# Kernel tuning notes

Hardware: AMD Instinct MI355X
Metric: run time of the kernel (lower is better)

## Reference

```python
import jax, jax.numpy as jnp
import numpy as np

HIDDEN_D = 1024
MAP_D = 2048


def lstm_cell(x, h, c, W_ih, W_hh, b_ih, b_hh):
    # PyTorch LSTMCell: gates ordered (i, f, g, o)
    gates = x @ W_ih.T + b_ih + h @ W_hh.T + b_hh  # [1, 4H]
    i, f, g, o = jnp.split(gates, 4, axis=-1)
    i = jax.nn.sigmoid(i)
    f = jax.nn.sigmoid(f)
    g = jnp.tanh(g)
    o = jax.nn.sigmoid(o)
    c_new = f * c + i * g
    h_new = o * jnp.tanh(c_new)
    return h_new, c_new


def setup_inputs() -> dict:
    key = jax.random.key(0)
    ks = jax.random.split(key, 16)
    H = HIDDEN_D
    s = 1.0 / np.sqrt(H)  # PyTorch LSTMCell init scale
    inp = {
        "goal_point": jax.random.normal(ks[0], (2,), jnp.float32),
        "current_point": jax.random.normal(ks[1], (2,), jnp.float32),
        "map": jax.random.normal(ks[2], (1, MAP_D), jnp.float32),
        # lstm_map: input_size = MAP_D
        "W_ih_map": jax.random.uniform(ks[3], (4 * H, MAP_D), jnp.float32, -s, s),
        "W_hh_map": jax.random.uniform(ks[4], (4 * H, H), jnp.float32, -s, s),
        "b_ih_map": jax.random.uniform(ks[5], (4 * H,), jnp.float32, -s, s),
        "b_hh_map": jax.random.uniform(ks[6], (4 * H,), jnp.float32, -s, s),
        # lstm_points: input_size = 4
        "W_ih_pts": jax.random.uniform(ks[7], (4 * H, 4), jnp.float32, -s, s),
        "W_hh_pts": jax.random.uniform(ks[8], (4 * H, H), jnp.float32, -s, s),
        "b_ih_pts": jax.random.uniform(ks[9], (4 * H,), jnp.float32, -s, s),
        "b_hh_pts": jax.random.uniform(ks[10], (4 * H,), jnp.float32, -s, s),
        # lstm1: input_size = 2H
        "W_ih_1": jax.random.uniform(ks[11], (4 * H, 2 * H), jnp.float32, -s, s),
        "W_hh_1": jax.random.uniform(ks[12], (4 * H, H), jnp.float32, -s, s),
        "b_ih_1": jax.random.uniform(ks[13], (4 * H,), jnp.float32, -s, s),
        "b_hh_1": jax.random.uniform(ks[14], (4 * H,), jnp.float32, -s, s),
        # fc: H -> 2
        "fc_w": jax.random.uniform(ks[15], (2, H), jnp.float32, -s, s),
        "fc_b": jnp.zeros((2,), jnp.float32),
    }
    return inp


def reference(goal_point, current_point, map,
              W_ih_map, W_hh_map, b_ih_map, b_hh_map,
              W_ih_pts, W_hh_pts, b_ih_pts, b_hh_pts,
              W_ih_1, W_hh_1, b_ih_1, b_hh_1,
              fc_w, fc_b):
    H = W_hh_map.shape[1]
    z = jnp.zeros((1, H), map.dtype)  # init_hidden: all-zero states
    points = jnp.concatenate([current_point, goal_point], axis=0)[None, :]  # [1, 4]

    h_map, _ = lstm_cell(map, z, z, W_ih_map, W_hh_map, b_ih_map, b_hh_map)
    h_pts, _ = lstm_cell(points, z, z, W_ih_pts, W_hh_pts, b_ih_pts, b_hh_pts)
    final_in = jnp.concatenate([h_map, h_pts], axis=1)  # [1, 2H]
    h1, _ = lstm_cell(final_in, z, z, W_ih_1, W_hh_1, b_ih_1, b_hh_1)
    # dropout disabled (deterministic reference / eval mode)
    output = h1 @ fc_w.T + fc_b  # [1, 2]
    return output
```

## Files before the change

### kernel.cpp

```cpp
#include <hip/hip_runtime.h>
#include <math.h>

#define H    1024
#define MAPD 2048

__device__ __forceinline__ float sigmoidf_(float x) {
    return 1.0f / (1.0f + expf(-x));
}

__device__ __forceinline__ float wave_reduce_sum(float v) {
#pragma unroll
    for (int off = 32; off >= 1; off >>= 1)
        v += __shfl_xor(v, off, 64);
    return v;
}

__global__ __launch_bounds__(256) void k_first(
    const float* __restrict__ x,
    const float* __restrict__ W,
    const float* __restrict__ b_ih,
    const float* __restrict__ b_hh,
    const float* __restrict__ Wp,
    const float* __restrict__ bp_ih,
    const float* __restrict__ bp_hh,
    const float* __restrict__ goal,
    const float* __restrict__ cur,
    float* __restrict__ fin)
{
    int b = blockIdx.x;
    if (b < 256) {
        int wave = threadIdx.x >> 6;
        int lane = threadIdx.x & 63;
        int j = b * 4 + wave;
        const float4* x4 = (const float4*)x;
        const float4* Wi = (const float4*)(W + (size_t)j * MAPD);
        const float4* Wg = (const float4*)(W + (size_t)(2 * H + j) * MAPD);
        const float4* Wo = (const float4*)(W + (size_t)(3 * H + j) * MAPD);
        float si = 0.f, sg = 0.f, so = 0.f;
#pragma unroll
        for (int it = 0; it < 8; ++it) {
            int idx = it * 64 + lane;
            float4 xv = x4[idx];
            float4 a = Wi[idx];
            si += a.x * xv.x + a.y * xv.y + a.z * xv.z + a.w * xv.w;
            float4 g = Wg[idx];
            sg += g.x * xv.x + g.y * xv.y + g.z * xv.z + g.w * xv.w;
            float4 o = Wo[idx];
            so += o.x * xv.x + o.y * xv.y + o.z * xv.z + o.w * xv.w;
        }
        si = wave_reduce_sum(si);
        sg = wave_reduce_sum(sg);
        so = wave_reduce_sum(so);
        if (lane == 0) {
            float gi = si + b_ih[j] + b_hh[j];
            float gg = sg + b_ih[2 * H + j] + b_hh[2 * H + j];
            float go = so + b_ih[3 * H + j] + b_hh[3 * H + j];
            float c = sigmoidf_(gi) * tanhf(gg);
            fin[j] = sigmoidf_(go) * tanhf(c);
        }
    } else {
        float p0 = cur[0], p1 = cur[1], p2 = goal[0], p3 = goal[1];
        const float4* Wp4 = (const float4*)Wp;
#pragma unroll
        for (int t = 0; t < 4; ++t) {
            int j = t * 256 + threadIdx.x;
            float4 wi = Wp4[j];
            float4 wg = Wp4[2 * H + j];
            float4 wo = Wp4[3 * H + j];
            float gi = wi.x * p0 + wi.y * p1 + wi.z * p2 + wi.w * p3 + bp_ih[j] + bp_hh[j];
            float gg = wg.x * p0 + wg.y * p1 + wg.z * p2 + wg.w * p3 + bp_ih[2 * H + j] + bp_hh[2 * H + j];
            float go = wo.x * p0 + wo.y * p1 + wo.z * p2 + wo.w * p3 + bp_ih[3 * H + j] + bp_hh[3 * H + j];
            float c = sigmoidf_(gi) * tanhf(gg);
            fin[H + j] = sigmoidf_(go) * tanhf(c);
        }
    }
}

__global__ __launch_bounds__(256) void k_lstm1(
    const float* __restrict__ fin,
    const float* __restrict__ W,
    const float* __restrict__ b_ih,
    const float* __restrict__ b_hh,
    float* __restrict__ h1)
{
    int wave = threadIdx.x >> 6;
    int lane = threadIdx.x & 63;
    int j = blockIdx.x * 4 + wave;
    const float4* x4 = (const float4*)fin;
    const float4* Wi = (const float4*)(W + (size_t)j * MAPD);
    const float4* Wg = (const float4*)(W + (size_t)(2 * H + j) * MAPD);
    const float4* Wo = (const float4*)(W + (size_t)(3 * H + j) * MAPD);
    float si = 0.f, sg = 0.f, so = 0.f;
#pragma unroll
    for (int it = 0; it < 8; ++it) {
        int idx = it * 64 + lane;
        float4 xv = x4[idx];
        float4 a = Wi[idx];
        si += a.x * xv.x + a.y * xv.y + a.z * xv.z + a.w * xv.w;
        float4 g = Wg[idx];
        sg += g.x * xv.x + g.y * xv.y + g.z * xv.z + g.w * xv.w;
        float4 o = Wo[idx];
        so += o.x * xv.x + o.y * xv.y + o.z * xv.z + o.w * xv.w;
    }
    si = wave_reduce_sum(si);
    sg = wave_reduce_sum(sg);
    so = wave_reduce_sum(so);
    if (lane == 0) {
        float gi = si + b_ih[j] + b_hh[j];
        float gg = sg + b_ih[2 * H + j] + b_hh[2 * H + j];
        float go = so + b_ih[3 * H + j] + b_hh[3 * H + j];
        float c = sigmoidf_(gi) * tanhf(gg);
        h1[j] = sigmoidf_(go) * tanhf(c);
    }
}

__global__ __launch_bounds__(128) void k_fc(
    const float* __restrict__ h1,
    const float* __restrict__ fcw,
    const float* __restrict__ fcb,
    float* __restrict__ out)
{
    int wave = threadIdx.x >> 6;
    int lane = threadIdx.x & 63;
    float s = 0.f;
#pragma unroll
    for (int k = 0; k < 16; ++k) {
        int idx = k * 64 + lane;
        s += h1[idx] * fcw[wave * H + idx];
    }
    s = wave_reduce_sum(s);
    if (lane == 0) out[wave] = s + fcb[wave];
}

extern "C" void kernel_launch(void* const* d_in, const int* in_sizes, int n_in,
                              void* d_out, int out_size, void* d_ws, size_t ws_size,
                              hipStream_t stream) {
    const float* goal    = (const float*)d_in[0];
    const float* cur     = (const float*)d_in[1];
    const float* map     = (const float*)d_in[2];
    const float* W_ih_map = (const float*)d_in[3];
    const float* b_ih_map = (const float*)d_in[5];
    const float* b_hh_map = (const float*)d_in[6];
    const float* W_ih_pts = (const float*)d_in[7];
    const float* b_ih_pts = (const float*)d_in[9];
    const float* b_hh_pts = (const float*)d_in[10];
    const float* W_ih_1  = (const float*)d_in[11];
    const float* b_ih_1  = (const float*)d_in[13];
    const float* b_hh_1  = (const float*)d_in[14];
    const float* fc_w    = (const float*)d_in[15];
    const float* fc_b    = (const float*)d_in[16];

    float* ws  = (float*)d_ws;
    float* out = (float*)d_out;

    k_first<<<257, 256, 0, stream>>>(map, W_ih_map, b_ih_map, b_hh_map,
                                     W_ih_pts, b_ih_pts, b_hh_pts,
                                     goal, cur, ws);
    k_lstm1<<<256, 256, 0, stream>>>(ws, W_ih_1, b_ih_1, b_hh_1, ws + 2048);
    k_fc<<<1, 128, 0, stream>>>(ws + 2048, fc_w, fc_b, out);
}
```

Measured before the change: 18.90 us.

## Fuse all three LSTM stages and FC into one cooperative kernel with grid sync

Replaces three kernel launches with a single cooperative kernel. Points-LSTM work is spread across all blocks, W_ih_1 rows are prefetched into registers before a grid-wide sync, and the FC layer is folded in through per-block atomicAdd onto a bias-initialized output. This removes launch gaps and overlaps the second weight load with the first stage. In exchange it adds cooperative launch overhead, a grid barrier, and register pressure from 24 float4 prefetch registers. The output initialization and the atomics are ordered only by the grid sync, so the result stays correct but floating-point summation order is nondeterministic.

```diff
diff --git a/kernel.cpp b/kernel.cpp
--- a/kernel.cpp
+++ b/kernel.cpp
@@ -1,41 +1,69 @@
 #include <hip/hip_runtime.h>
+#include <hip/hip_cooperative_groups.h>
 #include <math.h>
 
+namespace cg = cooperative_groups;
+
 #define H    1024
-#define MAPD 2048
+#define D2   2048
 
 __device__ __forceinline__ float sigmoidf_(float x) {
     return 1.0f / (1.0f + expf(-x));
 }
 
-__device__ __forceinline__ float wave_reduce_sum(float v) {
+__device__ __forceinline__ float wave_sum(float v) {
 #pragma unroll
     for (int off = 32; off >= 1; off >>= 1)
         v += __shfl_xor(v, off, 64);
     return v;
 }
 
-__global__ __launch_bounds__(256) void k_first(
+__global__ __launch_bounds__(256) void k_fused(
     const float* __restrict__ x,
-    const float* __restrict__ W,
-    const float* __restrict__ b_ih,
-    const float* __restrict__ b_hh,
+    const float* __restrict__ Wm,
+    const float* __restrict__ bm_i,
+    const float* __restrict__ bm_h,
     const float* __restrict__ Wp,
-    const float* __restrict__ bp_ih,
-    const float* __restrict__ bp_hh,
+    const float* __restrict__ bp_i,
+    const float* __restrict__ bp_h,
+    const float* __restrict__ W1,
+    const float* __restrict__ b1_i,
+    const float* __restrict__ b1_h,
     const float* __restrict__ goal,
     const float* __restrict__ cur,
-    float* __restrict__ fin)
+    const float* __restrict__ fcw,
+    const float* __restrict__ fcb,
+    float* __restrict__ fin,
+    float* __restrict__ out)
 {
-    int b = blockIdx.x;
-    if (b < 256) {
-        int wave = threadIdx.x >> 6;
-        int lane = threadIdx.x & 63;
-        int j = b * 4 + wave;
+    const int b    = blockIdx.x;
+    const int wave = threadIdx.x >> 6;
+    const int lane = threadIdx.x & 63;
+    const int j    = b * 4 + wave;
+
+    if (threadIdx.x < 4) {
+        int pj = b * 4 + threadIdx.x;
+        float p0 = cur[0], p1 = cur[1], p2 = goal[0], p3 = goal[1];
+        const float4* Wp4 = (const float4*)Wp;
+        float4 wi = Wp4[pj];
+        float4 wg = Wp4[2 * H + pj];
+        float4 wo = Wp4[3 * H + pj];
+        float gi = wi.x * p0 + wi.y * p1 + wi.z * p2 + wi.w * p3 + bp_i[pj] + bp_h[pj];
+        float gg = wg.x * p0 + wg.y * p1 + wg.z * p2 + wg.w * p3 + bp_i[2 * H + pj] + bp_h[2 * H + pj];
+        float go = wo.x * p0 + wo.y * p1 + wo.z * p2 + wo.w * p3 + bp_i[3 * H + pj] + bp_h[3 * H + pj];
+        float c = sigmoidf_(gi) * tanhf(gg);
+        fin[H + pj] = sigmoidf_(go) * tanhf(c);
+    }
+    if (b == 0 && threadIdx.x == 4) {
+        out[0] = fcb[0];
+        out[1] = fcb[1];
+    }
+
+    {
         const float4* x4 = (const float4*)x;
-        const float4* Wi = (const float4*)(W + (size_t)j * MAPD);
-        const float4* Wg = (const float4*)(W + (size_t)(2 * H + j) * MAPD);
-        const float4* Wo = (const float4*)(W + (size_t)(3 * H + j) * MAPD);
+        const float4* Wi = (const float4*)(Wm + (size_t)j * D2);
+        const float4* Wg = (const float4*)(Wm + (size_t)(2 * H + j) * D2);
+        const float4* Wo = (const float4*)(Wm + (size_t)(3 * H + j) * D2);
         float si = 0.f, sg = 0.f, so = 0.f;
 #pragma unroll
         for (int it = 0; it < 8; ++it) {
@@ -48,114 +76,97 @@
             float4 o = Wo[idx];
             so += o.x * xv.x + o.y * xv.y + o.z * xv.z + o.w * xv.w;
         }
-        si = wave_reduce_sum(si);
-        sg = wave_reduce_sum(sg);
-        so = wave_reduce_sum(so);
+        si = wave_sum(si);
+        sg = wave_sum(sg);
+        so = wave_sum(so);
         if (lane == 0) {
-            float gi = si + b_ih[j] + b_hh[j];
-            float gg = sg + b_ih[2 * H + j] + b_hh[2 * H + j];
-            float go = so + b_ih[3 * H + j] + b_hh[3 * H + j];
+            float gi = si + bm_i[j] + bm_h[j];
+            float gg = sg + bm_i[2 * H + j] + bm_h[2 * H + j];
+            float go = so + bm_i[3 * H + j] + bm_h[3 * H + j];
             float c = sigmoidf_(gi) * tanhf(gg);
             fin[j] = sigmoidf_(go) * tanhf(c);
         }
-    } else {
-        float p0 = cur[0], p1 = cur[1], p2 = goal[0], p3 = goal[1];
-        const float4* Wp4 = (const float4*)Wp;
+    }
+
+    float4 rA[8], rG[8], rO[8];
+    {
+        const float4* Vi = (const float4*)(W1 + (size_t)j * D2);
+        const float4* Vg = (const float4*)(W1 + (size_t)(2 * H + j) * D2);
+        const float4* Vo = (const float4*)(W1 + (size_t)(3 * H + j) * D2);
 #pragma unroll
-        for (int t = 0; t < 4; ++t) {
-            int j = t * 256 + threadIdx.x;
-            float4 wi = Wp4[j];
-            float4 wg = Wp4[2 * H + j];
-            float4 wo = Wp4[3 * H + j];
-            float gi = wi.x * p0 + wi.y * p1 + wi.z * p2 + wi.w * p3 + bp_ih[j] + bp_hh[j];
-            float gg = wg.x * p0 + wg.y * p1 + wg.z * p2 + wg.w * p3 + bp_ih[2 * H + j] + bp_hh[2 * H + j];
-            float go = wo.x * p0 + wo.y * p1 + wo.z * p2 + wo.w * p3 + bp_ih[3 * H + j] + bp_hh[3 * H + j];
-            float c = sigmoidf_(gi) * tanhf(gg);
-            fin[H + j] = sigmoidf_(go) * tanhf(c);
+        for (int it = 0; it < 8; ++it) {
+            int idx = it * 64 + lane;
+            rA[it] = Vi[idx];
+            rG[it] = Vg[idx];
+            rO[it] = Vo[idx];
         }
     }
-}
+    float fw0 = fcw[j], fw1 = fcw[H + j];
+    float bbi = b1_i[j] + b1_h[j];
+    float bbg = b1_i[2 * H + j] + b1_h[2 * H + j];
+    float bbo = b1_i[3 * H + j] + b1_h[3 * H + j];
 
-__global__ __launch_bounds__(256) void k_lstm1(
-    const float* __restrict__ fin,
-    const float* __restrict__ W,
-    const float* __restrict__ b_ih,
-    const float* __restrict__ b_hh,
-    float* __restrict__ h1)
-{
-    int wave = threadIdx.x >> 6;
-    int lane = threadIdx.x & 63;
-    int j = blockIdx.x * 4 + wave;
-    const float4* x4 = (const float4*)fin;
-    const float4* Wi = (const float4*)(W + (size_t)j * MAPD);
-    const float4* Wg = (const float4*)(W + (size_t)(2 * H + j) * MAPD);
-    const float4* Wo = (const float4*)(W + (size_t)(3 * H + j) * MAPD);
-    float si = 0.f, sg = 0.f, so = 0.f;
+    cg::this_grid().sync();
+
+    const float4* f4 = (const float4*)fin;
+    float ti = 0.f, tg = 0.f, to = 0.f;
 #pragma unroll
     for (int it = 0; it < 8; ++it) {
         int idx = it * 64 + lane;
-        float4 xv = x4[idx];
-        float4 a = Wi[idx];
-        si += a.x * xv.x + a.y * xv.y + a.z * xv.z + a.w * xv.w;
-        float4 g = Wg[idx];
-        sg += g.x * xv.x + g.y * xv.y + g.z * xv.z + g.w * xv.w;
-        float4 o = Wo[idx];
-        so += o.x * xv.x + o.y * xv.y + o.z * xv.z + o.w * xv.w;
+        float4 xv = f4[idx];
+        ti += rA[it].x * xv.x + rA[it].y * xv.y + rA[it].z * xv.z + rA[it].w * xv.w;
+        tg += rG[it].x * xv.x + rG[it].y * xv.y + rG[it].z * xv.z + rG[it].w * xv.w;
+        to += rO[it].x * xv.x + rO[it].y * xv.y + rO[it].z * xv.z + rO[it].w * xv.w;
     }
-    si = wave_reduce_sum(si);
-    sg = wave_reduce_sum(sg);
-    so = wave_reduce_sum(so);
+    ti = wave_sum(ti);
+    tg = wave_sum(tg);
+    to = wave_sum(to);
+
+    __shared__ float s0[4], s1[4];
     if (lane == 0) {
-        float gi = si + b_ih[j] + b_hh[j];
-        float gg = sg + b_ih[2 * H + j] + b_hh[2 * H + j];
-        float go = so + b_ih[3 * H + j] + b_hh[3 * H + j];
+        float gi = ti + bbi;
+        float gg = tg + bbg;
+        float go = to + bbo;
         float c = sigmoidf_(gi) * tanhf(gg);
-        h1[j] = sigmoidf_(go) * tanhf(c);
+        float h = sigmoidf_(go) * tanhf(c);
+        s0[wave] = h * fw0;
+        s1[wave] = h * fw1;
     }
-}
-
-__global__ __launch_bounds__(128) void k_fc(
-    const float* __restrict__ h1,
-    const float* __restrict__ fcw,
-    const float* __restrict__ fcb,
-    float* __restrict__ out)
-{
-    int wave = threadIdx.x >> 6;
-    int lane = threadIdx.x & 63;
-    float s = 0.f;
-#pragma unroll
-    for (int k = 0; k < 16; ++k) {
-        int idx = k * 64 + lane;
-        s += h1[idx] * fcw[wave * H + idx];
+    __syncthreads();
+    if (threadIdx.x == 0) {
+        atomicAdd(&out[0], s0[0] + s0[1] + s0[2] + s0[3]);
+        atomicAdd(&out[1], s1[0] + s1[1] + s1[2] + s1[3]);
     }
-    s = wave_reduce_sum(s);
-    if (lane == 0) out[wave] = s + fcb[wave];
 }
 
 extern "C" void kernel_launch(void* const* d_in, const int* in_sizes, int n_in,
                               void* d_out, int out_size, void* d_ws, size_t ws_size,
                               hipStream_t stream) {
-    const float* goal    = (const float*)d_in[0];
-    const float* cur     = (const float*)d_in[1];
-    const float* map     = (const float*)d_in[2];
+    const float* goal     = (const float*)d_in[0];
+    const float* cur      = (const float*)d_in[1];
+    const float* map      = (const float*)d_in[2];
     const float* W_ih_map = (const float*)d_in[3];
     const float* b_ih_map = (const float*)d_in[5];
     const float* b_hh_map = (const float*)d_in[6];
     const float* W_ih_pts = (const float*)d_in[7];
     const float* b_ih_pts = (const float*)d_in[9];
     const float* b_hh_pts = (const float*)d_in[10];
-    const float* W_ih_1  = (const float*)d_in[11];
-    const float* b_ih_1  = (const float*)d_in[13];
-    const float* b_hh_1  = (const float*)d_in[14];
-    const float* fc_w    = (const float*)d_in[15];
-    const float* fc_b    = (const float*)d_in[16];
+    const float* W_ih_1   = (const float*)d_in[11];
+    const float* b_ih_1   = (const float*)d_in[13];
+    const float* b_hh_1   = (const float*)d_in[14];
+    const float* fc_w     = (const float*)d_in[15];
+    const float* fc_b     = (const float*)d_in[16];
 
-    float* ws  = (float*)d_ws;
+    float* fin = (float*)d_ws;
     float* out = (float*)d_out;
 
-    k_first<<<257, 256, 0, stream>>>(map, W_ih_map, b_ih_map, b_hh_map,
-                                     W_ih_pts, b_ih_pts, b_hh_pts,
-                                     goal, cur, ws);
-    k_lstm1<<<256, 256, 0, stream>>>(ws, W_ih_1, b_ih_1, b_hh_1, ws + 2048);
-    k_fc<<<1, 128, 0, stream>>>(ws + 2048, fc_w, fc_b, out);
+    void* args[] = {
+        (void*)&map, (void*)&W_ih_map, (void*)&b_ih_map, (void*)&b_hh_map,
+        (void*)&W_ih_pts, (void*)&b_ih_pts, (void*)&b_hh_pts,
+        (void*)&W_ih_1, (void*)&b_ih_1, (void*)&b_hh_1,
+        (void*)&goal, (void*)&cur, (void*)&fc_w, (void*)&fc_b,
+        (void*)&fin, (void*)&out
+    };
+    hipLaunchCooperativeKernel((const void*)k_fused, dim3(256), dim3(256),
+                               args, 0, stream);
 }
```

Result: slower. 62.89 us (+232.7%).
